# Optimization experiments

Measured on AMD Instinct MI355X. Metric: run time of the kernel, lower is better.

Reference implementation:

```python
import jax, jax.numpy as jnp
import numpy as np

N, E, IN, HID, OUT = 8192, 262144, 3000, 256, 64
EPS = 1e-5


def setup_inputs() -> dict:
    key = jax.random.key(0)
    k = jax.random.split(key, 16)
    s = lambda i, shp, sc: jax.random.normal(k[i], shp, jnp.float32) * sc
    return {
        "feat": s(0, (N, IN), 1.0),
        "feat_a": s(1, (N, IN), 1.0),
        "graph_neigh": jax.random.uniform(k[2], (N, N), jnp.float32),
        "W1": s(3, (IN, HID), (1.0 / IN) ** 0.5),
        "att_src": s(4, (HID,), (1.0 / HID) ** 0.5),
        "att_dst": s(5, (HID,), (1.0 / HID) ** 0.5),
        "W2": s(6, (HID, OUT), (1.0 / HID) ** 0.5),
        "Wd1": s(7, (OUT, HID), (1.0 / OUT) ** 0.5),
        "bd1": jnp.zeros((HID,), jnp.float32),
        "gamma": jnp.ones((HID,), jnp.float32),
        "beta": jnp.zeros((HID,), jnp.float32),
        "Wd2": s(8, (HID, IN), (1.0 / HID) ** 0.5),
        "bd2": jnp.zeros((IN,), jnp.float32),
        "disc_W": s(9, (OUT, OUT), (1.0 / OUT) ** 0.5),
        "disc_b": jnp.zeros((), jnp.float32),
        "edge_index": jax.random.randint(k[10], (2, E), 0, N),
    }


def _gat_conv1(x, W1, att_src, att_dst, src, dst):
    # GATConv, heads=1, concat=False, no self-loops, no bias
    h = x @ W1                                    # [N, HID]
    a_src = h @ att_src                           # [N]
    a_dst = h @ att_dst                           # [N]
    e = jax.nn.leaky_relu(a_src[src] + a_dst[dst], 0.2)   # [E]
    m = jax.ops.segment_max(e, dst, num_segments=N)
    p = jnp.exp(e - m[dst])
    z = jax.ops.segment_sum(p, dst, num_segments=N)
    alpha = p / (z[dst] + 1e-16)                  # segment softmax over in-edges
    return jax.ops.segment_sum(alpha[:, None] * h[src], dst, num_segments=N)


def _encode(x, W1, att_src, att_dst, W2, src, dst):
    h1 = jax.nn.elu(_gat_conv1(x, W1, att_src, att_dst, src, dst))
    # conv2 is invoked with attention=False -> GraphST GATConv returns only lin(x) (heads=1 mean)
    return h1 @ W2


def _decoder(h, Wd1, bd1, gamma, beta, Wd2, bd2):
    z = h @ Wd1 + bd1
    mu = z.mean(0)
    var = z.var(0)  # biased, matches torch BN training normalization
    z = (z - mu) * jax.lax.rsqrt(var + EPS) * gamma + beta
    z = jax.nn.elu(z)
    return z @ Wd2 + bd2


def _readout(h, mask):
    vsum = mask @ h                               # [N, OUT]
    g = vsum / mask.sum(1, keepdims=True)
    g = g / jnp.clip(jnp.linalg.norm(g, axis=1, keepdims=True), 1e-12)
    return jax.nn.sigmoid(g)


def reference(feat, feat_a, graph_neigh, W1, att_src, att_dst, W2, Wd1, bd1,
              gamma, beta, Wd2, bd2, disc_W, disc_b, edge_index):
    src, dst = edge_index[0], edge_index[1]
    h2 = _encode(feat, W1, att_src, att_dst, W2, src, dst)
    h2_a = _encode(feat_a, W1, att_src, att_dst, W2, src, dst)
    h3 = _decoder(h2, Wd1, bd1, gamma, beta, Wd2, bd2)
    g = _readout(h2, graph_neigh)
    g_a = _readout(h2_a, graph_neigh)

    def disc(c, hp, hm):
        sc1 = jnp.einsum('nd,de,ne->n', hp, disc_W, c) + disc_b
        sc2 = jnp.einsum('nd,de,ne->n', hm, disc_W, c) + disc_b
        return jnp.stack([sc1, sc2], axis=1)

    ret = disc(g, h2, h2_a)
    ret_a = disc(g_a, h2_a, h2)
    return (h2, h3, ret, ret_a, h2, h2_a)
```

## Files before the change

### kernel.cpp

```cpp
#include <hip/hip_runtime.h>
#include <hip/hip_bf16.h>
#include <math.h>

constexpr int NN  = 8192;
constexpr int EE  = 262144;
constexpr int IN  = 3000;
constexpr int INP = 3008;
constexpr int HID = 256;
constexpr int OUT = 64;

constexpr long O_H2   = 0;
constexpr long O_H3   = 524288;
constexpr long O_RET  = 25100288;
constexpr long O_RETA = 25116672;
constexpr long O_H2B  = 25133056;
constexpr long O_H2A  = 25657344;

typedef __attribute__((ext_vector_type(8))) short short8v;
typedef __attribute__((ext_vector_type(4))) float f32x4;

__device__ __forceinline__ short f2bf(float f) {
    unsigned u = __float_as_uint(f);
    return (short)((u + 0x7FFF + ((u >> 16) & 1)) >> 16);
}
__device__ __forceinline__ float bf2f(unsigned short u) {
    return __uint_as_float(((unsigned)u) << 16);
}

__global__ void cvt_featK(const float* __restrict__ x, unsigned short* __restrict__ xb) {
    long i = (long)blockIdx.x * 256 + threadIdx.x;
    int r = (int)(i / 376), c8 = (int)(i % 376) * 8;
    short8v v;
    if (c8 + 8 <= IN) {
        const float* xr = x + (long)r * IN + c8;
        float4 v0 = *reinterpret_cast<const float4*>(xr);
        float4 v1 = *reinterpret_cast<const float4*>(xr + 4);
        v[0]=f2bf(v0.x); v[1]=f2bf(v0.y); v[2]=f2bf(v0.z); v[3]=f2bf(v0.w);
        v[4]=f2bf(v1.x); v[5]=f2bf(v1.y); v[6]=f2bf(v1.z); v[7]=f2bf(v1.w);
    } else {
#pragma unroll
        for (int j = 0; j < 8; ++j)
            v[j] = (c8 + j < IN) ? f2bf(x[(long)r * IN + c8 + j]) : (short)0;
    }
    *reinterpret_cast<short8v*>(xb + (long)r * INP + c8) = v;
}

__global__ void cvt_W1t(const float* __restrict__ W, unsigned short* __restrict__ Wt) {
    int i = blockIdx.x * 256 + threadIdx.x;
    int n = i / INP, k = i % INP;
    Wt[i] = (k < IN) ? (unsigned short)f2bf(W[(long)k * HID + n]) : 0;
}

__global__ void cvt_W2t(const float* __restrict__ W, unsigned short* __restrict__ Wt) {
    int i = blockIdx.x * 256 + threadIdx.x;
    int n = i / HID, k = i % HID;
    Wt[i] = (unsigned short)f2bf(W[(long)k * OUT + n]);
}

__global__ void cvt_Wd1t(const float* __restrict__ W, unsigned short* __restrict__ Wt) {
    int i = blockIdx.x * 256 + threadIdx.x;
    int n = i / OUT, k = i % OUT;
    Wt[i] = (unsigned short)f2bf(W[(long)k * HID + n]);
}

__global__ void cvt_Wd2t(const float* __restrict__ W, unsigned short* __restrict__ Wt) {
    int i = blockIdx.x * 256 + threadIdx.x;
    int n = i / HID, k = i % HID;
    Wt[i] = (n < IN) ? (unsigned short)f2bf(W[(long)k * IN + n]) : 0;
}

__global__ __launch_bounds__(256) void mfma_gemm_bf(const unsigned short* __restrict__ A,
                                                    const unsigned short* __restrict__ Bt,
                                                    const float* __restrict__ bias,
                                                    float* __restrict__ C,
                                                    unsigned short* __restrict__ Cb,
                                                    int M, int N, int Kp) {
    __shared__ unsigned short As[64][72];
    __shared__ unsigned short Bs[64][72];
    int t = threadIdx.x, w = t >> 6, l = t & 63;
    int row0 = blockIdx.y * 64, col0 = blockIdx.x * 64;
    int srow = t >> 2, scol = (t & 3) * 16;
    const unsigned short* Ap = A  + (long)(row0 + srow) * Kp + scol;
    const unsigned short* Bp = Bt + (long)(col0 + srow) * Kp + scol;
    int wm = (w >> 1) * 32, wn = (w & 1) * 32;
    int fr = l & 15, fq = l >> 4;
    int nk = Kp >> 6;

    short8v a0r, a1r, b0r, b1r;
    a0r = *reinterpret_cast<const short8v*>(Ap);
    a1r = *reinterpret_cast<const short8v*>(Ap + 8);
    b0r = *reinterpret_cast<const short8v*>(Bp);
    b1r = *reinterpret_cast<const short8v*>(Bp + 8);

    f32x4 acc[2][2] = {};
    for (int tt = 0; tt < nk; ++tt) {
        *reinterpret_cast<short8v*>(&As[srow][scol])     = a0r;
        *reinterpret_cast<short8v*>(&As[srow][scol + 8]) = a1r;
        *reinterpret_cast<short8v*>(&Bs[srow][scol])     = b0r;
        *reinterpret_cast<short8v*>(&Bs[srow][scol + 8]) = b1r;
        __syncthreads();
        if (tt + 1 < nk) {
            const unsigned short* Ap2 = Ap + (tt + 1) * 64;
            const unsigned short* Bp2 = Bp + (tt + 1) * 64;
            a0r = *reinterpret_cast<const short8v*>(Ap2);
            a1r = *reinterpret_cast<const short8v*>(Ap2 + 8);
            b0r = *reinterpret_cast<const short8v*>(Bp2);
            b1r = *reinterpret_cast<const short8v*>(Bp2 + 8);
        }
#pragma unroll
        for (int kk = 0; kk < 2; ++kk) {
            short8v fa0 = *reinterpret_cast<const short8v*>(&As[wm + fr][kk * 32 + fq * 8]);
            short8v fa1 = *reinterpret_cast<const short8v*>(&As[wm + 16 + fr][kk * 32 + fq * 8]);
            short8v fb0 = *reinterpret_cast<const short8v*>(&Bs[wn + fr][kk * 32 + fq * 8]);
            short8v fb1 = *reinterpret_cast<const short8v*>(&Bs[wn + 16 + fr][kk * 32 + fq * 8]);
            acc[0][0] = __builtin_amdgcn_mfma_f32_16x16x32_bf16(fa0, fb0, acc[0][0], 0, 0, 0);
            acc[0][1] = __builtin_amdgcn_mfma_f32_16x16x32_bf16(fa0, fb1, acc[0][1], 0, 0, 0);
            acc[1][0] = __builtin_amdgcn_mfma_f32_16x16x32_bf16(fa1, fb0, acc[1][0], 0, 0, 0);
            acc[1][1] = __builtin_amdgcn_mfma_f32_16x16x32_bf16(fa1, fb1, acc[1][1], 0, 0, 0);
        }
        __syncthreads();
    }
    int dc = l & 15;
#pragma unroll
    for (int i = 0; i < 2; ++i)
#pragma unroll
        for (int j = 0; j < 2; ++j) {
            int c = col0 + wn + j * 16 + dc;
            if (c < N) {
                float bb = bias ? bias[c] : 0.f;
#pragma unroll
                for (int q = 0; q < 4; ++q) {
                    int r = row0 + wm + i * 16 + fq * 4 + q;
                    float v = acc[i][j][q] + bb;
                    long idx = (long)r * N + c;
                    if (C)  C[idx]  = v;
                    if (Cb) Cb[idx] = (unsigned short)f2bf(v);
                }
            }
        }
}

__global__ __launch_bounds__(256) void readout_mfma2(const float* __restrict__ gn,
                                                     const unsigned short* __restrict__ HT,
                                                     float* __restrict__ vsum_part,
                                                     float* __restrict__ rowsum_part) {
    __shared__ unsigned short As[64][72];
    __shared__ unsigned short Bs[128][72];
    __shared__ float rsacc[64][4];
    int t = threadIdx.x, w = t >> 6, l = t & 63;
    int row0 = blockIdx.x * 64;
    int kc = blockIdx.y, kbeg = kc * 2048;
    int asr = t >> 2, asc = (t & 3) * 16;
    int bsr = t >> 1, bsc = (t & 1) * 32;
    const float*          Ap = gn + (long)(row0 + asr) * NN + kbeg + asc;
    const unsigned short* Bp = HT + (long)bsr * NN + kbeg + bsc;
    int wm = (w >> 1) * 32, wn = (w & 1) * 64;
    int fr = l & 15, fq = l >> 4;

    float4  a4[4];
    short8v b8[4];
#pragma unroll
    for (int q = 0; q < 4; ++q) a4[q] = *reinterpret_cast<const float4*>(Ap + q * 4);
#pragma unroll
    for (int q = 0; q < 4; ++q) b8[q] = *reinterpret_cast<const short8v*>(Bp + q * 8);

    f32x4 acc[2][4] = {};
    float myrs = 0.f;
    for (int it = 0; it < 32; ++it) {
#pragma unroll
        for (int q = 0; q < 4; ++q) {
            float4 v = a4[q];
            ushort4 s;
            s.x = (unsigned short)f2bf(v.x);
            s.y = (unsigned short)f2bf(v.y);
            s.z = (unsigned short)f2bf(v.z);
            s.w = (unsigned short)f2bf(v.w);
            *reinterpret_cast<ushort4*>(&As[asr][asc + q * 4]) = s;
            myrs += v.x + v.y + v.z + v.w;
        }
#pragma unroll
        for (int q = 0; q < 4; ++q)
            *reinterpret_cast<short8v*>(&Bs[bsr][bsc + q * 8]) = b8[q];
        __syncthreads();
        if (it + 1 < 32) {
            const float*          Ap2 = Ap + (it + 1) * 64;
            const unsigned short* Bp2 = Bp + (it + 1) * 64;
#pragma unroll
            for (int q = 0; q < 4; ++q) a4[q] = *reinterpret_cast<const float4*>(Ap2 + q * 4);
#pragma unroll
            for (int q = 0; q < 4; ++q) b8[q] = *reinterpret_cast<const short8v*>(Bp2 + q * 8);
        }
#pragma unroll
        for (int kk = 0; kk < 2; ++kk) {
            short8v fa0 = *reinterpret_cast<const short8v*>(&As[wm + fr][kk * 32 + fq * 8]);
            short8v fa1 = *reinterpret_cast<const short8v*>(&As[wm + 16 + fr][kk * 32 + fq * 8]);
#pragma unroll
            for (int j = 0; j < 4; ++j) {
                short8v fb = *reinterpret_cast<const short8v*>(&Bs[wn + j * 16 + fr][kk * 32 + fq * 8]);
                acc[0][j] = __builtin_amdgcn_mfma_f32_16x16x32_bf16(fa0, fb, acc[0][j], 0, 0, 0);
                acc[1][j] = __builtin_amdgcn_mfma_f32_16x16x32_bf16(fa1, fb, acc[1][j], 0, 0, 0);
            }
        }
        __syncthreads();
    }
    rsacc[asr][t & 3] = myrs;
    __syncthreads();
    if (t < 64)
        rowsum_part[(long)kc * NN + row0 + t] =
            rsacc[t][0] + rsacc[t][1] + rsacc[t][2] + rsacc[t][3];
    int dc = l & 15;
#pragma unroll
    for (int i = 0; i < 2; ++i)
#pragma unroll
        for (int j = 0; j < 4; ++j) {
            int c = wn + j * 16 + dc;
#pragma unroll
            for (int q = 0; q < 4; ++q) {
                int r = row0 + wm + i * 16 + fq * 4 + q;
                vsum_part[((long)kc * NN + r) * 128 + c] = acc[i][j][q];
            }
        }
}

__global__ void deg_count(const int* __restrict__ dst, int* __restrict__ deg) {
    int i = blockIdx.x * 256 + threadIdx.x;
    if (i < EE) atomicAdd(&deg[dst[i]], 1);
}

__global__ __launch_bounds__(256) void scan_offsets(const int* __restrict__ deg,
                                                    int* __restrict__ off,
                                                    int* __restrict__ cursor) {
    __shared__ int part[256];
    int t = threadIdx.x;
    int base = t * 32;
    int local[32];
    int s = 0;
#pragma unroll
    for (int i = 0; i < 32; ++i) { local[i] = s; s += deg[base + i]; }
    part[t] = s;
    __syncthreads();
    for (int o2 = 1; o2 < 256; o2 <<= 1) {
        int v = (t >= o2) ? part[t - o2] : 0;
        __syncthreads();
        part[t] += v;
        __syncthreads();
    }
    int pre = (t == 0) ? 0 : part[t - 1];
#pragma unroll
    for (int i = 0; i < 32; ++i) {
        int v = pre + local[i];
        off[base + i] = v;
        cursor[base + i] = v;
    }
}

__global__ void scatter_edges(const int* __restrict__ src, const int* __restrict__ dst,
                              int* __restrict__ cursor, int* __restrict__ ssrc) {
    int i = blockIdx.x * 256 + threadIdx.x;
    if (i >= EE) return;
    int slot = atomicAdd(&cursor[dst[i]], 1);
    ssrc[slot] = src[i];
}

__global__ void attn_coeff_bf(const unsigned short* __restrict__ h,
                              const float* __restrict__ att_src,
                              const float* __restrict__ att_dst,
                              float* __restrict__ a_src, float* __restrict__ a_dst) {
    int wave = threadIdx.x >> 6, lane = threadIdx.x & 63;
    int n = blockIdx.x * 4 + wave;
    ushort4 hv = *reinterpret_cast<const ushort4*>(&h[(long)n * HID + lane * 4]);
    float4 vs = *reinterpret_cast<const float4*>(&att_src[lane * 4]);
    float4 vd = *reinterpret_cast<const float4*>(&att_dst[lane * 4]);
    float h0 = bf2f(hv.x), h1 = bf2f(hv.y), h2v = bf2f(hv.z), h3v = bf2f(hv.w);
    float s1 = h0 * vs.x + h1 * vs.y + h2v * vs.z + h3v * vs.w;
    float s2 = h0 * vd.x + h1 * vd.y + h2v * vd.z + h3v * vd.w;
#pragma unroll
    for (int off = 32; off > 0; off >>= 1) {
        s1 += __shfl_down(s1, off);
        s2 += __shfl_down(s2, off);
    }
    if (lane == 0) { a_src[n] = s1; a_dst[n] = s2; }
}

__global__ __launch_bounds__(256) void gat_gather(const int* __restrict__ ssrc,
                                                  const int* __restrict__ off,
                                                  const int* __restrict__ deg,
                                                  const float* __restrict__ asrc,
                                                  const float* __restrict__ adst,
                                                  const unsigned short* __restrict__ h,
                                                  unsigned short* __restrict__ gat) {
    int wv = threadIdx.x >> 6, lane = threadIdx.x & 63;
    int d = blockIdx.x * 4 + wv;
    int o = off[d], n = deg[d];
    float ad = adst[d];

    float m = -INFINITY;
    for (int j = lane; j < n; j += 64) {
        float e = asrc[ssrc[o + j]] + ad;
        e = e > 0.f ? e : 0.2f * e;
        m = fmaxf(m, e);
    }
#pragma unroll
    for (int t = 32; t; t >>= 1) m = fmaxf(m, __shfl_xor(m, t));
    float z = 0.f;
    for (int j = lane; j < n; j += 64) {
        float e = asrc[ssrc[o + j]] + ad;
        e = e > 0.f ? e : 0.2f * e;
        z += expf(e - m);
    }
#pragma unroll
    for (int t = 32; t; t >>= 1) z += __shfl_xor(z, t);
    float zinv = 1.0f / (z + 1e-16f);

    float4 acc = {0.f, 0.f, 0.f, 0.f};
    int j = 0;
    for (; j + 2 <= n; j += 2) {
        int s0 = ssrc[o + j], s1 = ssrc[o + j + 1];
        const ushort4 h0 = *reinterpret_cast<const ushort4*>(&h[(long)s0 * HID + lane * 4]);
        const ushort4 h1 = *reinterpret_cast<const ushort4*>(&h[(long)s1 * HID + lane * 4]);
        float e0 = asrc[s0] + ad; e0 = e0 > 0.f ? e0 : 0.2f * e0;
        float e1 = asrc[s1] + ad; e1 = e1 > 0.f ? e1 : 0.2f * e1;
        float a0 = expf(e0 - m) * zinv;
        float a1 = expf(e1 - m) * zinv;
        acc.x += a0 * bf2f(h0.x) + a1 * bf2f(h1.x);
        acc.y += a0 * bf2f(h0.y) + a1 * bf2f(h1.y);
        acc.z += a0 * bf2f(h0.z) + a1 * bf2f(h1.z);
        acc.w += a0 * bf2f(h0.w) + a1 * bf2f(h1.w);
    }
    if (j < n) {
        int s0 = ssrc[o + j];
        const ushort4 h0 = *reinterpret_cast<const ushort4*>(&h[(long)s0 * HID + lane * 4]);
        float e0 = asrc[s0] + ad; e0 = e0 > 0.f ? e0 : 0.2f * e0;
        float a0 = expf(e0 - m) * zinv;
        acc.x += a0 * bf2f(h0.x); acc.y += a0 * bf2f(h0.y);
        acc.z += a0 * bf2f(h0.z); acc.w += a0 * bf2f(h0.w);
    }
    ushort4 r;
    r.x = (unsigned short)f2bf(acc.x > 0.f ? acc.x : expm1f(acc.x));
    r.y = (unsigned short)f2bf(acc.y > 0.f ? acc.y : expm1f(acc.y));
    r.z = (unsigned short)f2bf(acc.z > 0.f ? acc.z : expm1f(acc.z));
    r.w = (unsigned short)f2bf(acc.w > 0.f ? acc.w : expm1f(acc.w));
    *reinterpret_cast<ushort4*>(&gat[(long)d * HID + lane * 4]) = r;
}

__global__ void bn_partial(const float* __restrict__ zd, float* __restrict__ s,
                           float* __restrict__ sq) {
    int t = threadIdx.x;
    float a = 0.f, b = 0.f;
    int r0 = blockIdx.x * 128;
    for (int r = r0; r < r0 + 128; ++r) {
        float v = zd[(long)r * HID + t];
        a += v;
        b += v * v;
    }
    atomicAdd(&s[t], a);
    atomicAdd(&sq[t], b);
}

__global__ void bn_finalize(const float* __restrict__ s, const float* __restrict__ sq,
                            const float* __restrict__ gamma, const float* __restrict__ beta,
                            float* __restrict__ scale, float* __restrict__ shift) {
    int t = threadIdx.x;
    float mean = s[t] / (float)NN;
    float var  = sq[t] / (float)NN - mean * mean;
    float sc   = gamma[t] * rsqrtf(var + 1e-5f);
    scale[t] = sc;
    shift[t] = beta[t] - mean * sc;
}

__global__ void bn_apply_elu_bf(const float* __restrict__ zd, const float* __restrict__ scale,
                                const float* __restrict__ shift, unsigned short* __restrict__ zb) {
    for (long i = (long)blockIdx.x * blockDim.x + threadIdx.x; i < (long)NN * HID;
         i += (long)gridDim.x * blockDim.x) {
        int c = (int)(i & 255);
        float v = zd[i] * scale[c] + shift[c];
        v = v > 0.f ? v : expm1f(v);
        zb[i] = (unsigned short)f2bf(v);
    }
}

__global__ void pack_hcatT(const float* __restrict__ h2, const float* __restrict__ h2a,
                           unsigned short* __restrict__ HT) {
    int c = blockIdx.x;
    int r = blockIdx.y * 256 + threadIdx.x;
    float v = (c < 64) ? h2[(long)r * 64 + c] : h2a[(long)r * 64 + (c - 64)];
    HT[(long)c * NN + r] = (unsigned short)f2bf(v);
}

__global__ void readout_norm2(const float* __restrict__ vsum_part,
                              const float* __restrict__ rowsum_part,
                              float* __restrict__ g, float* __restrict__ ga) {
    int r = blockIdx.x;
    int c = threadIdx.x;
    float v = 0.f;
#pragma unroll
    for (int kc = 0; kc < 4; ++kc)
        v += vsum_part[((long)kc * NN + r) * 128 + c];
    float rs = 0.f;
#pragma unroll
    for (int kc = 0; kc < 4; ++kc)
        rs += rowsum_part[(long)kc * NN + r];
    v /= rs;
    int w = c >> 6, lane = c & 63;
    float sq = v * v;
#pragma unroll
    for (int off = 32; off > 0; off >>= 1) sq += __shfl_xor(sq, off);
    float nrm = fmaxf(sqrtf(sq), 1e-12f);
    float out = 1.0f / (1.0f + expf(-(v / nrm)));
    (w == 0 ? g : ga)[(long)r * 64 + lane] = out;
}

__global__ void disc_kernel(const float* __restrict__ h2, const float* __restrict__ h2a,
                            const float* __restrict__ g, const float* __restrict__ ga,
                            const float* __restrict__ W, const float* __restrict__ b,
                            float* __restrict__ ret, float* __restrict__ reta) {
    int n = blockIdx.x;
    int w = threadIdx.x >> 6, lane = threadIdx.x & 63;
    const float* c = (w == 0) ? g : ga;
    float u = 0.f;
#pragma unroll 8
    for (int e = 0; e < 64; ++e) u += W[lane * 64 + e] * c[(long)n * 64 + e];
    float hp = ((w == 0) ? h2 : h2a)[(long)n * 64 + lane];
    float hm = ((w == 0) ? h2a : h2)[(long)n * 64 + lane];
    float t1 = hp * u, t2 = hm * u;
    for (int off = 32; off > 0; off >>= 1) {
        t1 += __shfl_xor(t1, off);
        t2 += __shfl_xor(t2, off);
    }
    if (lane == 0) {
        float bb = b[0];
        if (w == 0) { ret[n * 2] = t1 + bb;  ret[n * 2 + 1] = t2 + bb; }
        else        { reta[n * 2] = t1 + bb; reta[n * 2 + 1] = t2 + bb; }
    }
}

__global__ void copy_h2(const float* __restrict__ h2, const float* __restrict__ h2a,
                        float* __restrict__ out) {
    int i = blockIdx.x * 256 + threadIdx.x;
    float v = h2[i], va = h2a[i];
    out[O_H2 + i]  = v;
    out[O_H2B + i] = v;
    out[O_H2A + i] = va;
}

extern "C" void kernel_launch(void* const* d_in, const int* in_sizes, int n_in,
                              void* d_out, int out_size, void* d_ws, size_t ws_size,
                              hipStream_t stream) {
    const float* feat    = (const float*)d_in[0];
    const float* feat_a  = (const float*)d_in[1];
    const float* gneigh  = (const float*)d_in[2];
    const float* W1      = (const float*)d_in[3];
    const float* att_src = (const float*)d_in[4];
    const float* att_dst = (const float*)d_in[5];
    const float* W2      = (const float*)d_in[6];
    const float* Wd1     = (const float*)d_in[7];
    const float* bd1     = (const float*)d_in[8];
    const float* gamma   = (const float*)d_in[9];
    const float* beta    = (const float*)d_in[10];
    const float* Wd2     = (const float*)d_in[11];
    const float* bd2     = (const float*)d_in[12];
    const float* disc_W  = (const float*)d_in[13];
    const float* disc_b  = (const float*)d_in[14];
    const int*   eidx    = (const int*)d_in[15];
    const int*   src = eidx;
    const int*   dst = eidx + EE;
    float* out = (float*)d_out;

    float* w = (float*)d_ws;
    float* h_buf   = w;
    unsigned short* h_bf = (unsigned short*)h_buf;
    unsigned short* gat_bf = (unsigned short*)(h_buf + 2097152);
    float* zdec    = h_buf + 2097152 + 1048576;
    unsigned short* zdec_bf = (unsigned short*)(zdec + 2097152);
    float* h2      = zdec + 2097152 + 1048576;
    float* h2a     = h2 + 524288;
    float* gbuf    = h2a + 524288;
    float* gabuf   = gbuf + 524288;
    unsigned short* h2b = (unsigned short*)(gabuf + 524288);
    float* asrc    = gabuf + 524288 + 262144;
    float* adst    = asrc + 8192;
    float* bnsum   = adst + 8192;
    float* bnsq    = bnsum + 256;
    float* scale   = bnsq + 256;
    float* shift   = scale + 256;
    unsigned short* W1t  = (unsigned short*)(shift + 256);
    unsigned short* W2t  = W1t + 770048;
    unsigned short* Wd1t = W2t + 16384;
    unsigned short* Wd2t = Wd1t + 16384;
    int*   ideg    = (int*)(Wd2t + 770048);
    int*   ioff    = ideg + 8192;
    int*   icur    = ioff + 8192;
    int*   issrc   = icur + 8192;
    float* vsum_part = h_buf;
    unsigned short* HT = zdec_bf;
    float* rowsum_part = ((float*)zdec_bf) + 524288;
    unsigned short* fb = (unsigned short*)(out + O_H3);

    cvt_W1t<<<3008, 256, 0, stream>>>(W1, W1t);
    cvt_W2t<<<64, 256, 0, stream>>>(W2, W2t);
    cvt_Wd1t<<<64, 256, 0, stream>>>(Wd1, Wd1t);
    cvt_Wd2t<<<3008, 256, 0, stream>>>(Wd2, Wd2t);

    hipMemsetAsync(ideg, 0, 8192 * 4, stream);
    deg_count<<<EE / 256, 256, 0, stream>>>(dst, ideg);
    scan_offsets<<<1, 256, 0, stream>>>(ideg, ioff, icur);
    scatter_edges<<<EE / 256, 256, 0, stream>>>(src, dst, icur, issrc);

    auto encode_pass = [&](const float* x, float* h2_out) {
        cvt_featK<<<12032, 256, 0, stream>>>(x, fb);
        mfma_gemm_bf<<<dim3(4, 128), 256, 0, stream>>>(fb, W1t, nullptr,
                                                       nullptr, h_bf, NN, HID, INP);
        attn_coeff_bf<<<2048, 256, 0, stream>>>(h_bf, att_src, att_dst, asrc, adst);
        gat_gather<<<2048, 256, 0, stream>>>(issrc, ioff, ideg, asrc, adst, h_bf, gat_bf);
        mfma_gemm_bf<<<dim3(1, 128), 256, 0, stream>>>(gat_bf, W2t, nullptr,
                                                       h2_out, h2b, NN, OUT, HID);
    };

    encode_pass(feat, h2);
    float* h2b_keep_marker = nullptr; (void)h2b_keep_marker;
    encode_pass(feat_a, h2a);
    {
    }
    extern __global__ void cvt_h2b_decl();
    void(0);
    {
        struct L { static __global__ void k(const float* __restrict__ a,
                                            unsigned short* __restrict__ b) {
            int i = blockIdx.x * 256 + threadIdx.x;
            b[i] = (unsigned short)f2bf(a[i]);
        }};
        L::k<<<2048, 256, 0, stream>>>(h2, h2b);
    }
    mfma_gemm_bf<<<dim3(4, 128), 256, 0, stream>>>(h2b, Wd1t, bd1,
                                                   zdec, nullptr, NN, HID, OUT);
    hipMemsetAsync(bnsum, 0, 512 * 4, stream);
    bn_partial<<<64, 256, 0, stream>>>(zdec, bnsum, bnsq);
    bn_finalize<<<1, 256, 0, stream>>>(bnsum, bnsq, gamma, beta, scale, shift);
    bn_apply_elu_bf<<<2048, 256, 0, stream>>>(zdec, scale, shift, zdec_bf);
    mfma_gemm_bf<<<dim3(47, 128), 256, 0, stream>>>(zdec_bf, Wd2t, bd2,
                                                    out + O_H3, nullptr, NN, IN, HID);

    pack_hcatT<<<dim3(128, 32), 256, 0, stream>>>(h2, h2a, HT);
    readout_mfma2<<<dim3(128, 4), 256, 0, stream>>>(gneigh, HT, vsum_part, rowsum_part);
    readout_norm2<<<8192, 128, 0, stream>>>(vsum_part, rowsum_part, gbuf, gabuf);

    disc_kernel<<<8192, 128, 0, stream>>>(h2, h2a, gbuf, gabuf, disc_W, disc_b,
                                          out + O_RET, out + O_RETA);

    copy_h2<<<2048, 256, 0, stream>>>(h2, h2a, out);
}
```

Measured before the change: 435.9 us.

## Fuse fp32-to-bf16 feature conversion into a 128x128 split-K encoder GEMM

Replaces the separate feature-to-bf16 conversion kernel with a templated 128x128-tile MFMA GEMM that reads fp32 features directly, converts them in registers, and prefetches the next K tile while the current one computes. The encoder GEMM is split along K into two chunks that write fp32 partials, and a new kernel sums them and emits the bf16 hidden activations. The decoder output GEMM also moves to the 128x128 kernel, with the Wd2 transpose padded to 3072 columns to cover the last tile. This avoids a full write and reread of the bf16 feature copy and enlarges tiles for more reuse, at the cost of partial-sum traffic, an extra reduce launch, and higher register pressure.

```diff
diff --git a/kernel.cpp b/kernel.cpp
--- a/kernel.cpp
+++ b/kernel.cpp
@@ -27,46 +27,164 @@
     return __uint_as_float(((unsigned)u) << 16);
 }
 
-__global__ void cvt_featK(const float* __restrict__ x, unsigned short* __restrict__ xb) {
-    long i = (long)blockIdx.x * 256 + threadIdx.x;
-    int r = (int)(i / 376), c8 = (int)(i % 376) * 8;
-    short8v v;
-    if (c8 + 8 <= IN) {
-        const float* xr = x + (long)r * IN + c8;
-        float4 v0 = *reinterpret_cast<const float4*>(xr);
-        float4 v1 = *reinterpret_cast<const float4*>(xr + 4);
-        v[0]=f2bf(v0.x); v[1]=f2bf(v0.y); v[2]=f2bf(v0.z); v[3]=f2bf(v0.w);
-        v[4]=f2bf(v1.x); v[5]=f2bf(v1.y); v[6]=f2bf(v1.z); v[7]=f2bf(v1.w);
-    } else {
-#pragma unroll
-        for (int j = 0; j < 8; ++j)
-            v[j] = (c8 + j < IN) ? f2bf(x[(long)r * IN + c8 + j]) : (short)0;
-    }
-    *reinterpret_cast<short8v*>(xb + (long)r * INP + c8) = v;
-}
-
 __global__ void cvt_W1t(const float* __restrict__ W, unsigned short* __restrict__ Wt) {
     int i = blockIdx.x * 256 + threadIdx.x;
     int n = i / INP, k = i % INP;
     Wt[i] = (k < IN) ? (unsigned short)f2bf(W[(long)k * HID + n]) : 0;
 }
-
 __global__ void cvt_W2t(const float* __restrict__ W, unsigned short* __restrict__ Wt) {
     int i = blockIdx.x * 256 + threadIdx.x;
     int n = i / HID, k = i % HID;
     Wt[i] = (unsigned short)f2bf(W[(long)k * OUT + n]);
 }
-
 __global__ void cvt_Wd1t(const float* __restrict__ W, unsigned short* __restrict__ Wt) {
     int i = blockIdx.x * 256 + threadIdx.x;
     int n = i / OUT, k = i % OUT;
     Wt[i] = (unsigned short)f2bf(W[(long)k * HID + n]);
 }
-
 __global__ void cvt_Wd2t(const float* __restrict__ W, unsigned short* __restrict__ Wt) {
     int i = blockIdx.x * 256 + threadIdx.x;
     int n = i / HID, k = i % HID;
     Wt[i] = (n < IN) ? (unsigned short)f2bf(W[(long)k * IN + n]) : 0;
+}
+__global__ void cvt_f2b(const float* __restrict__ a, unsigned short* __restrict__ b) {
+    int i = blockIdx.x * 256 + threadIdx.x;
+    b[i] = (unsigned short)f2bf(a[i]);
+}
+
+template<int AF32>
+__global__ __launch_bounds__(256) void mfma_gemm128(const void* __restrict__ Av,
+                                                    const unsigned short* __restrict__ Bt,
+                                                    const float* __restrict__ bias,
+                                                    float* __restrict__ Cf,
+                                                    float* __restrict__ Cpart,
+                                                    int M, int N, int lda, int ldb, int aK,
+                                                    int tilesPerChunk, int totalTiles) {
+    __shared__ unsigned short As[128][72];
+    __shared__ unsigned short Bs[128][72];
+    int t = threadIdx.x, w = t >> 6, l = t & 63;
+    int row0 = blockIdx.y * 128, col0 = blockIdx.x * 128;
+    int sr = t >> 1, sh = (t & 1) * 32;
+    int wm = (w >> 1) * 64, wn = (w & 1) * 64;
+    int fr = l & 15, fq = l >> 4;
+    int kbeg = blockIdx.z * tilesPerChunk * 64;
+    int ktiles = min(tilesPerChunk, totalTiles - blockIdx.z * tilesPerChunk);
+
+    const float*          Af = (const float*)Av;
+    const unsigned short* Ab = (const unsigned short*)Av;
+    const unsigned short* Bp = Bt + (long)(col0 + sr) * ldb + sh;
+
+    float4  paf[8];
+    short8v pab[4];
+    short8v pb[4];
+
+    auto loadA = [&](int k0) {
+        if (AF32) {
+            const float* Ar = Af + (long)(row0 + sr) * lda + k0 + sh;
+            if (k0 + 64 <= aK) {
+#pragma unroll
+                for (int q = 0; q < 8; ++q) paf[q] = *reinterpret_cast<const float4*>(Ar + q * 4);
+            } else {
+#pragma unroll
+                for (int q = 0; q < 8; ++q) {
+                    float4 v;
+                    int kb = k0 + sh + q * 4;
+                    v.x = (kb + 0 < aK) ? Ar[q * 4 + 0] : 0.f;
+                    v.y = (kb + 1 < aK) ? Ar[q * 4 + 1] : 0.f;
+                    v.z = (kb + 2 < aK) ? Ar[q * 4 + 2] : 0.f;
+                    v.w = (kb + 3 < aK) ? Ar[q * 4 + 3] : 0.f;
+                    paf[q] = v;
+                }
+            }
+        } else {
+            const unsigned short* Ar = Ab + (long)(row0 + sr) * lda + k0 + sh;
+#pragma unroll
+            for (int q = 0; q < 4; ++q) pab[q] = *reinterpret_cast<const short8v*>(Ar + q * 8);
+        }
+    };
+    auto loadB = [&](int k0) {
+#pragma unroll
+        for (int q = 0; q < 4; ++q) pb[q] = *reinterpret_cast<const short8v*>(Bp + k0 + q * 8);
+    };
+
+    loadA(kbeg);
+    loadB(kbeg);
+
+    f32x4 acc[4][4] = {};
+    for (int tt = 0; tt < ktiles; ++tt) {
+        if (AF32) {
+#pragma unroll
+            for (int q = 0; q < 4; ++q) {
+                float4 v0 = paf[q * 2], v1 = paf[q * 2 + 1];
+                short8v s;
+                s[0]=f2bf(v0.x); s[1]=f2bf(v0.y); s[2]=f2bf(v0.z); s[3]=f2bf(v0.w);
+                s[4]=f2bf(v1.x); s[5]=f2bf(v1.y); s[6]=f2bf(v1.z); s[7]=f2bf(v1.w);
+                *reinterpret_cast<short8v*>(&As[sr][sh + q * 8]) = s;
+            }
+        } else {
+#pragma unroll
+            for (int q = 0; q < 4; ++q)
+                *reinterpret_cast<short8v*>(&As[sr][sh + q * 8]) = pab[q];
+        }
+#pragma unroll
+        for (int q = 0; q < 4; ++q)
+            *reinterpret_cast<short8v*>(&Bs[sr][sh + q * 8]) = pb[q];
+        __syncthreads();
+        if (tt + 1 < ktiles) {
+            int k0 = kbeg + (tt + 1) * 64;
+            loadA(k0);
+            loadB(k0);
+        }
+#pragma unroll
+        for (int kk = 0; kk < 2; ++kk) {
+            short8v fa[4], fb[4];
+#pragma unroll
+            for (int i = 0; i < 4; ++i)
+                fa[i] = *reinterpret_cast<const short8v*>(&As[wm + i * 16 + fr][kk * 32 + fq * 8]);
+#pragma unroll
+            for (int j = 0; j < 4; ++j)
+                fb[j] = *reinterpret_cast<const short8v*>(&Bs[wn + j * 16 + fr][kk * 32 + fq * 8]);
+#pragma unroll
+            for (int i = 0; i < 4; ++i)
+#pragma unroll
+                for (int j = 0; j < 4; ++j)
+                    acc[i][j] = __builtin_amdgcn_mfma_f32_16x16x32_bf16(fa[i], fb[j], acc[i][j], 0, 0, 0);
+        }
+        __syncthreads();
+    }
+    int dc = l & 15;
+#pragma unroll
+    for (int i = 0; i < 4; ++i)
+#pragma unroll
+        for (int j = 0; j < 4; ++j) {
+            int c = col0 + wn + j * 16 + dc;
+            if (Cpart) {
+#pragma unroll
+                for (int q = 0; q < 4; ++q) {
+                    int r = row0 + wm + i * 16 + fq * 4 + q;
+                    Cpart[((long)blockIdx.z * M + r) * N + c] = acc[i][j][q];
+                }
+            } else if (c < N) {
+                float bb = bias ? bias[c] : 0.f;
+#pragma unroll
+                for (int q = 0; q < 4; ++q) {
+                    int r = row0 + wm + i * 16 + fq * 4 + q;
+                    Cf[(long)r * N + c] = acc[i][j][q] + bb;
+                }
+            }
+        }
+}
+
+__global__ void reduce_cvt(const float* __restrict__ p, unsigned short* __restrict__ hb) {
+    int i4 = (blockIdx.x * 256 + threadIdx.x) * 4;
+    float4 a = *reinterpret_cast<const float4*>(p + i4);
+    float4 b = *reinterpret_cast<const float4*>(p + 2097152 + i4);
+    ushort4 r;
+    r.x = (unsigned short)f2bf(a.x + b.x);
+    r.y = (unsigned short)f2bf(a.y + b.y);
+    r.z = (unsigned short)f2bf(a.z + b.z);
+    r.w = (unsigned short)f2bf(a.w + b.w);
+    *reinterpret_cast<ushort4*>(hb + i4) = r;
 }
 
 __global__ __launch_bounds__(256) void mfma_gemm_bf(const unsigned short* __restrict__ A,
@@ -487,19 +605,19 @@
     unsigned short* W2t  = W1t + 770048;
     unsigned short* Wd1t = W2t + 16384;
     unsigned short* Wd2t = Wd1t + 16384;
-    int*   ideg    = (int*)(Wd2t + 770048);
+    int*   ideg    = (int*)(Wd2t + 786432);
     int*   ioff    = ideg + 8192;
     int*   icur    = ioff + 8192;
     int*   issrc   = icur + 8192;
+    float* part = w + 2097152;
     float* vsum_part = h_buf;
     unsigned short* HT = zdec_bf;
     float* rowsum_part = ((float*)zdec_bf) + 524288;
-    unsigned short* fb = (unsigned short*)(out + O_H3);
 
     cvt_W1t<<<3008, 256, 0, stream>>>(W1, W1t);
     cvt_W2t<<<64, 256, 0, stream>>>(W2, W2t);
     cvt_Wd1t<<<64, 256, 0, stream>>>(Wd1, Wd1t);
-    cvt_Wd2t<<<3008, 256, 0, stream>>>(Wd2, Wd2t);
+    cvt_Wd2t<<<3072, 256, 0, stream>>>(Wd2, Wd2t);
 
     hipMemsetAsync(ideg, 0, 8192 * 4, stream);
     deg_count<<<EE / 256, 256, 0, stream>>>(dst, ideg);
@@ -507,9 +625,9 @@
     scatter_edges<<<EE / 256, 256, 0, stream>>>(src, dst, icur, issrc);
 
     auto encode_pass = [&](const float* x, float* h2_out) {
-        cvt_featK<<<12032, 256, 0, stream>>>(x, fb);
-        mfma_gemm_bf<<<dim3(4, 128), 256, 0, stream>>>(fb, W1t, nullptr,
-                                                       nullptr, h_bf, NN, HID, INP);
+        mfma_gemm128<1><<<dim3(2, 64, 2), 256, 0, stream>>>(
+            x, W1t, nullptr, nullptr, part, NN, HID, IN, INP, IN, 24, 47);
+        reduce_cvt<<<2048, 256, 0, stream>>>(part, h_bf);
         attn_coeff_bf<<<2048, 256, 0, stream>>>(h_bf, att_src, att_dst, asrc, adst);
         gat_gather<<<2048, 256, 0, stream>>>(issrc, ioff, ideg, asrc, adst, h_bf, gat_bf);
         mfma_gemm_bf<<<dim3(1, 128), 256, 0, stream>>>(gat_bf, W2t, nullptr,
@@ -517,28 +635,17 @@
     };
 
     encode_pass(feat, h2);
-    float* h2b_keep_marker = nullptr; (void)h2b_keep_marker;
     encode_pass(feat_a, h2a);
-    {
-    }
-    extern __global__ void cvt_h2b_decl();
-    void(0);
-    {
-        struct L { static __global__ void k(const float* __restrict__ a,
-                                            unsigned short* __restrict__ b) {
-            int i = blockIdx.x * 256 + threadIdx.x;
-            b[i] = (unsigned short)f2bf(a[i]);
-        }};
-        L::k<<<2048, 256, 0, stream>>>(h2, h2b);
-    }
+    cvt_f2b<<<2048, 256, 0, stream>>>(h2, h2b);
+
     mfma_gemm_bf<<<dim3(4, 128), 256, 0, stream>>>(h2b, Wd1t, bd1,
                                                    zdec, nullptr, NN, HID, OUT);
     hipMemsetAsync(bnsum, 0, 512 * 4, stream);
     bn_partial<<<64, 256, 0, stream>>>(zdec, bnsum, bnsq);
     bn_finalize<<<1, 256, 0, stream>>>(bnsum, bnsq, gamma, beta, scale, shift);
     bn_apply_elu_bf<<<2048, 256, 0, stream>>>(zdec, scale, shift, zdec_bf);
-    mfma_gemm_bf<<<dim3(47, 128), 256, 0, stream>>>(zdec_bf, Wd2t, bd2,
-                                                    out + O_H3, nullptr, NN, IN, HID);
+    mfma_gemm128<0><<<dim3(24, 64, 1), 256, 0, stream>>>(
+        zdec_bf, Wd2t, bd2, out + O_H3, nullptr, NN, IN, HID, HID, HID, 4, 4);
 
     pack_hcatT<<<dim3(128, 32), 256, 0, stream>>>(h2, h2a, HT);
     readout_mfma2<<<dim3(128, 4), 256, 0, stream>>>(gneigh, HT, vsum_part, rowsum_part);
```

After: 449.8 us. 1.03x slower.
